# Optimization experiments

Measured on AMD Instinct MI355X. Metric: run time of the kernel, lower is better.

The kernel has to match this reference:

```python
import jax, jax.numpy as jnp
import numpy as np
from jax import lax

B, NAV, HIM, WIM, RH, NF, AE = 16, 36, 120, 160, 512, 4, 37
TEMP = 10.0  # __init__ overrides softmax_temperature to 10
DN = ('NCHW', 'OIHW', 'NCHW')


def _conv(x, w, b, stride, pad, dil, groups):
    y = lax.conv_general_dilated(x, w, window_strides=stride,
                                 padding=[(pad[0], pad[0]), (pad[1], pad[1])],
                                 rhs_dilation=dil, dimension_numbers=DN,
                                 feature_group_count=groups)
    return y + b[None, :, None, None]


def _avgpool(x, k, s):
    y = lax.reduce_window(x, 0.0, lax.add, (1, 1) + k, (1, 1) + s, 'VALID')
    return y / float(k[0] * k[1])


def _conv2_path(x, w1, b1, w2, b2):
    # conv2_1 -> avgpool(3,3) -> conv2_2 -> avgpool(3,9); output [B,3,12]
    y = _conv(x, w1, b1, (5, 7), (0, 0), (10, 10), 1)
    y = _avgpool(y, (3, 3), (3, 3))
    y = _conv(y, w2, b2, (2, 2), (0, 0), (1, 2), 1)
    y = _avgpool(y, (3, 9), (3, 3))
    return y[:, 0]  # squeeze channel -> [B,3,12]


def setup_inputs() -> dict:
    key = jax.random.key(0)
    ks = jax.random.split(key, 24)
    p = lambda k, shape, s=0.02: (jax.random.normal(k, shape) * s).astype(jnp.float32)
    inp = {
        'depth_raw': jax.random.uniform(ks[0], (B, NAV, HIM, WIM), jnp.float32),
        'depth_clip': jax.random.uniform(ks[1], (B, NAV, HIM, WIM), jnp.float32),
        'obj_feat': jax.random.uniform(ks[2], (B, NAV, HIM, WIM), jnp.float32),
        'num_navigable_feat': jax.random.uniform(ks[3], (B, NAV), jnp.float32),
        'pre_action_feat': jax.random.normal(ks[4], (B, AE), jnp.float32),
        'h_0': jax.random.normal(ks[5], (B, RH), jnp.float32),
        'c_0': jax.random.normal(ks[6], (B, RH), jnp.float32),
        'weighted_ctx': jax.random.normal(ks[7], (B, RH), jnp.float32),
        'navigable_index': jax.random.randint(ks[8], (B, 8), 0, NAV),
        # conv1: grouped Conv2d(72 -> 36, k=5, pad=2, groups=36)
        'conv1_w': p(ks[9], (NAV, 2, 5, 5)),
        'conv1_b': p(ks[10], (NAV,)),
        # Dynamic_conv2d: MLP ctx -> filter attention + bank of 4 grouped-filter sets
        'dyn_fc1_w': p(ks[11], (RH // 4, RH)),
        'dyn_fc1_b': p(ks[12], (RH // 4,)),
        'dyn_fc2_w': p(ks[13], (NF, RH // 4)),
        'dyn_fc2_b': p(ks[14], (NF,)),
        'dyn_filters': p(ks[15], (NF, NAV, 2, 5, 5)),
        # conv2_1 / conv2_2: 1->1 channel convs
        'conv2_1_w': p(ks[16], (1, 1, 5, 5)),
        'conv2_1_b': p(ks[17], (1,)),
        'conv2_2_w': p(ks[18], (1, 1, 3, 3)),
        'conv2_2_b': p(ks[19], (1,)),
        # LSTMCell(input=RH+NAV+NF+AE, hidden=RH); gates ordered i,f,g,o
        'lstm_w_ih': p(ks[20], (4 * RH, RH + NAV + NF + AE)),
        'lstm_w_hh': p(ks[21], (4 * RH, RH)),
        'lstm_b_ih': p(ks[22], (4 * RH,)),
        'lstm_b_hh': p(ks[23], (4 * RH,)),
    }
    return inp


def reference(depth_raw, depth_clip, obj_feat, num_navigable_feat, pre_action_feat,
              h_0, c_0, weighted_ctx, navigable_index,
              conv1_w, conv1_b, dyn_fc1_w, dyn_fc1_b, dyn_fc2_w, dyn_fc2_b, dyn_filters,
              conv2_1_w, conv2_1_b, conv2_2_w, conv2_2_b,
              lstm_w_ih, lstm_w_hh, lstm_b_ih, lstm_b_hh):
    # interleave raw/clip depth channels: [B,36,2,H,W] -> [B,72,H,W]
    mtf1 = jnp.stack((depth_raw, depth_clip), axis=2).reshape(B, 2 * NAV, HIM, WIM)
    total_depth = _conv(mtf1, conv1_w, conv1_b, (1, 1), (2, 2), (1, 1), NAV)  # [B,36,H,W]

    attn = jax.nn.softmax(num_navigable_feat, axis=1)  # [B,36]
    pd = total_depth * attn[:, :, None, None]
    po = obj_feat * attn[:, :, None, None]
    mtf2 = jnp.stack((pd, po), axis=2).reshape(B, 2 * NAV, HIM, WIM)

    # dynamic filter conv: ctx-conditioned mixture of filter banks
    hid = jax.nn.relu(weighted_ctx @ dyn_fc1_w.T + dyn_fc1_b)
    dfa = jax.nn.softmax(hid @ dyn_fc2_w.T + dyn_fc2_b, axis=1)  # [B,4]
    kern = jnp.einsum('bf,foikl->boikl', dfa, dyn_filters)  # [B,36,2,5,5]

    def one_sample(xb, kb):
        return lax.conv_general_dilated(xb[None], kb, (1, 1), [(2, 2), (2, 2)],
                                        dimension_numbers=DN,
                                        feature_group_count=NAV)[0]

    tvf = jax.vmap(one_sample)(mtf2, kern)  # [B,36,H,W]

    # panorama assembly: dir i -> row (2 - i//12), col (i%12)
    pano = tvf.reshape(B, 3, 12, HIM, WIM)[:, ::-1]
    pano = pano.transpose(0, 1, 3, 2, 4).reshape(B, 1, 3 * HIM, 12 * WIM)

    vf1 = _conv2_path(pano, conv2_1_w, conv2_1_b, conv2_2_w, conv2_2_b)
    vf2 = _conv2_path(jnp.roll(pano, WIM, axis=3), conv2_1_w, conv2_1_b, conv2_2_w, conv2_2_b)
    vf2 = jnp.roll(vf2, -1, axis=-1)
    vf = (vf1 + vf2) * 0.5
    vf = vf[:, ::-1].reshape(B, NAV)  # flip rows then flatten
    vf = jax.nn.softmax(vf / TEMP, axis=1)

    nav_mask = jnp.zeros((B, NAV), jnp.float32).at[jnp.arange(B)[:, None], navigable_index].set(1.0)

    concat = jnp.concatenate((weighted_ctx, vf, dfa, pre_action_feat), axis=1)
    gates = concat @ lstm_w_ih.T + lstm_b_ih + h_0 @ lstm_w_hh.T + lstm_b_hh
    i, f, g, o = jnp.split(gates, 4, axis=1)
    c_1 = jax.nn.sigmoid(f) * c_0 + jax.nn.sigmoid(i) * jnp.tanh(g)
    h_1 = jax.nn.sigmoid(o) * jnp.tanh(c_1)
    return (h_1, c_1, vf, nav_mask)
```

## Files before the change

kernel.cpp:

```cpp
#include <hip/hip_runtime.h>
#include <math.h>

#define B 16
#define NAV 36
#define HIM 120
#define WIM 160
#define RH 512
#define NF 4
#define AE 37


__global__ __launch_bounds__(128) void k_head(
    const float* __restrict__ nnf, const float* __restrict__ ctx,
    const float* __restrict__ fc1w, const float* __restrict__ fc1b,
    const float* __restrict__ fc2w, const float* __restrict__ fc2b,
    float* __restrict__ attn, float* __restrict__ dfa) {
  int b = blockIdx.x;
  int t = threadIdx.x;
  __shared__ float s_ctx[RH];
  __shared__ float s_v[NAV];
  __shared__ float s_hid[128];
  __shared__ float s_l[NF];
  __shared__ float s_inv[2];

  if (t < NAV) s_v[t] = nnf[b * NAV + t];
  for (int k = t; k < RH; k += 128) s_ctx[k] = ctx[b * RH + k];
  __syncthreads();

  if (t == 0) {
    float m = -1e30f;
    for (int i = 0; i < NAV; i++) m = fmaxf(m, s_v[i]);
    float s = 0.f;
    for (int i = 0; i < NAV; i++) { s_v[i] = expf(s_v[i] - m); s += s_v[i]; }
    s_inv[0] = 1.0f / s;
  }
  float acc = fc1b[t];
  const float* wr = fc1w + t * RH;
  for (int k = 0; k < RH; k++) acc += s_ctx[k] * wr[k];
  s_hid[t] = fmaxf(acc, 0.0f);
  __syncthreads();

  if (t < NAV) attn[b * NAV + t] = s_v[t] * s_inv[0];
  if (t < NF) {
    float a = fc2b[t];
    const float* w2 = fc2w + t * 128;
    for (int k = 0; k < 128; k++) a += s_hid[k] * w2[k];
    s_l[t] = a;
  }
  __syncthreads();
  if (t == 0) {
    float m = fmaxf(fmaxf(s_l[0], s_l[1]), fmaxf(s_l[2], s_l[3]));
    float s = 0.f;
    for (int f = 0; f < NF; f++) { s_l[f] = expf(s_l[f] - m); s += s_l[f]; }
    s_inv[1] = 1.0f / s;
  }
  __syncthreads();
  if (t < NF) dfa[b * NF + t] = s_l[t] * s_inv[1];
}

__global__ __launch_bounds__(192) void k_comp(
    const float* __restrict__ c1w, const float* __restrict__ c1b,
    const float* __restrict__ dynf,
    const float* __restrict__ attn, const float* __restrict__ dfa,
    float* __restrict__ wsC) {
  int bi = blockIdx.x;
  int b = bi / NAV, i = bi - b * NAV;
  int t = threadIdx.x;
  __shared__ float s_kd[50];
  __shared__ float s_w1[50];
  if (t < 50) {
    float a = 0.f;
    for (int f = 0; f < NF; f++) a += dfa[b * NF + f] * dynf[(f * NAV + i) * 50 + t];
    s_kd[t] = a;
    s_w1[t] = c1w[i * 50 + t];
  }
  __syncthreads();
  float attn_bi = attn[bi];
  float* o = wsC + (size_t)bi * 240;
  if (t < 162) {
    int ch = t < 81 ? 0 : 1;
    int uv = t - 81 * ch;
    int u = uv / 9, v = uv - 9 * u;
    float c = 0.f;
    for (int a = 0; a < 5; a++) {
      int cc = u - a; if (cc < 0 || cc > 4) continue;
      for (int bb = 0; bb < 5; bb++) {
        int d = v - bb; if (d < 0 || d > 4) continue;
        c += s_kd[a * 5 + bb] * s_w1[ch * 25 + cc * 5 + d];
      }
    }
    o[ch * 81 + uv] = c * attn_bi;
  } else if (t < 187) {
    o[t] = s_kd[25 + (t - 162)] * attn_bi;
  } else if (t == 187) {
    float s2 = 0.f;
    for (int j = 0; j < 25; j++) s2 += s_kd[j];
    o[187] = attn_bi * c1b[i] * s2;
  }
  if (t < 50) o[188 + t] = s_kd[t];
}

#define LDW 172
__global__ __launch_bounds__(512) void k_conv(
    const float* __restrict__ draw, const float* __restrict__ dclip,
    const float* __restrict__ obj,
    const float* __restrict__ wsC,
    float* __restrict__ cpano) {
  __shared__ __align__(16) float s_raw[24 * LDW];
  __shared__ __align__(16) float s_clip[24 * LDW];
  __shared__ __align__(16) float s_po[20 * LDW];
  __shared__ __align__(16) float s_part[1920];
  __shared__ float s_C[188];

  int t = threadIdx.x;
  int bz = blockIdx.x;
  int half = bz & 1;
  int pi = bz >> 1;
  int b = pi / NAV, i = pi - b * NAV;
  int ybase = 60 * half;

  const size_t plane = (size_t)pi * HIM * WIM;
  const float* rawp = draw + plane;
  const float* clipp = dclip + plane;
  const float* objp = obj + plane;
  int q = i / 12, cw = i - 12 * q;
  float* cpb = cpano + ((size_t)b * 72 + (2 - q) * 24) * 1920 + cw * WIM;

  const float* cp = wsC + (size_t)pi * 240;
  if (t < 188) s_C[t] = cp[t];
  if (t < 384) {
    int ha = t < 192 ? 0 : 1, rem = t - 192 * ha;
    int r = rem >> 3, hc = rem & 7;
    int col = hc < 4 ? hc : 160 + hc;
    (ha ? s_clip : s_raw)[r * LDW + col] = 0.f;
  }
  if (t < 160) {
    int r = t >> 3, hc = t & 7;
    int col = hc < 4 ? hc : 160 + hc;
    s_po[r * LDW + col] = 0.f;
  }

  int prow[2], pg3[2]; bool pra[2];
#pragma unroll
  for (int jj = 0; jj < 2; jj++) {
    int idx = t + 512 * jj;
    pra[jj] = idx < 960;
    prow[jj] = idx / 40;
    pg3[jj] = idx - 40 * prow[jj];
  }
  int vrow[2], vg[2]; bool va[2];
#pragma unroll
  for (int jj = 0; jj < 2; jj++) {
    int idx = t + 512 * jj;
    va[jj] = idx < 800;
    vrow[jj] = idx / 40;
    vg[jj] = idx - 40 * vrow[jj];
  }
  int part = t / 160;
  int pgc = t - 160 * part;
  int row4 = pgc / 40;
  int gc = pgc - 40 * row4;
  int x0 = 4 * gc;
  int rbase = 5 * row4;
  bool cact = (t < 480);
  int rrow4 = t / 40;
  int rg = t - 40 * rrow4;

  for (int tt = 0; tt < 3; tt++) {
    int y0 = ybase + 20 * tt;
    {
      float4 vr[2], vc[2], vo[2];
#pragma unroll
      for (int jj = 0; jj < 2; jj++) {
        int gy = y0 - 4 + prow[jj];
        bool ok = pra[jj] && gy >= 0 && gy < HIM;
        float4 a = {0.f, 0.f, 0.f, 0.f}, c = {0.f, 0.f, 0.f, 0.f};
        if (ok) { a = *(const float4*)(rawp + gy * WIM + 4 * pg3[jj]);
                  c = *(const float4*)(clipp + gy * WIM + 4 * pg3[jj]); }
        vr[jj] = a; vc[jj] = c;
      }
#pragma unroll
      for (int jj = 0; jj < 2; jj++) {
        int gy = y0 - 2 + vrow[jj];
        float4 v = {0.f, 0.f, 0.f, 0.f};
        if (va[jj] && gy >= 0 && gy < HIM)
          v = *(const float4*)(objp + gy * WIM + 4 * vg[jj]);
        vo[jj] = v;
      }
#pragma unroll
      for (int jj = 0; jj < 2; jj++) {
        if (pra[jj]) {
          *(float4*)&s_raw[prow[jj] * LDW + 4 + 4 * pg3[jj]] = vr[jj];
          *(float4*)&s_clip[prow[jj] * LDW + 4 + 4 * pg3[jj]] = vc[jj];
        }
      }
#pragma unroll
      for (int jj = 0; jj < 2; jj++) {
        if (va[jj]) *(float4*)&s_po[vrow[jj] * LDW + 4 + 4 * vg[jj]] = vo[jj];
      }
    }
    __syncthreads();

    if (cact) {
      float a0 = 0.f, a1 = 0.f, a2 = 0.f, a3 = 0.f;
      int ub = rbase + 3 * part;
#pragma unroll
      for (int u = 0; u < 3; u++) {
        const float* rp = &s_raw[(ub + u) * LDW + x0];
        const float* cl = &s_clip[(ub + u) * LDW + x0];
        float rw[12], cc[12];
        *(float4*)&rw[0] = *(const float4*)rp;
        *(float4*)&rw[4] = *(const float4*)(rp + 4);
        *(float4*)&rw[8] = *(const float4*)(rp + 8);
        *(float4*)&cc[0] = *(const float4*)cl;
        *(float4*)&cc[4] = *(const float4*)(cl + 4);
        *(float4*)&cc[8] = *(const float4*)(cl + 8);
        const float* Cr = &s_C[(3 * part + u) * 9];
#pragma unroll
        for (int v = 0; v < 9; v++) {
          float wr = Cr[v], wc = Cr[81 + v];
          a0 += rw[v] * wr + cc[v] * wc;
          a1 += rw[v + 1] * wr + cc[v + 1] * wc;
          a2 += rw[v + 2] * wr + cc[v + 2] * wc;
          a3 += rw[v + 3] * wr + cc[v + 3] * wc;
        }
      }
      int ndd = (part == 2) ? 1 : 2;
      int dd0 = 2 * part;
      for (int dd = 0; dd < ndd; dd++) {
        int dr = dd0 + dd;
        const float* pp = &s_po[(rbase + dr) * LDW + x0];
        float po[12];
        *(float4*)&po[0] = *(const float4*)pp;
        *(float4*)&po[4] = *(const float4*)(pp + 4);
        *(float4*)&po[8] = *(const float4*)(pp + 8);
        const float* Cp = &s_C[162 + dr * 5];
#pragma unroll
        for (int d = 0; d < 5; d++) {
          float w = Cp[d];
          a0 += po[d + 2] * w;
          a1 += po[d + 3] * w;
          a2 += po[d + 4] * w;
          a3 += po[d + 5] * w;
        }
      }
      float4 p4 = {a0, a1, a2, a3};
      *(float4*)&s_part[t * 4] = p4;
    }
    __syncthreads();

    if (t < 160) {
      float4 p0 = *(const float4*)&s_part[(0 * 160 + t) * 4];
      float4 p1 = *(const float4*)&s_part[(1 * 160 + t) * 4];
      float4 p2 = *(const float4*)&s_part[(2 * 160 + t) * 4];
      float c187 = s_C[187];
      float a0 = p0.x + p1.x + p2.x + c187;
      float a1 = p0.y + p1.y + p2.y + c187;
      float a2 = p0.z + p1.z + p2.z + c187;
      float a3 = p0.w + p1.w + p2.w + c187;
      int y = y0 + 5 * rrow4;
      if (y != 0) {
        float* op = cpb + (size_t)(12 * half + 4 * tt + rrow4) * 1920 + 4 * rg;
        if (rg == 0) { op[2] = a2; op[3] = a3; }
        else if (rg == 39) { op[0] = a0; op[1] = a1; }
        else { float4 o4 = {a0, a1, a2, a3}; *(float4*)op = o4; }
      }
    }
  }
}

__global__ __launch_bounds__(256) void k_fix(
    const float* __restrict__ draw, const float* __restrict__ dclip,
    const float* __restrict__ obj,
    const float* __restrict__ c1w, const float* __restrict__ c1b,
    const float* __restrict__ attn, const float* __restrict__ wsC,
    float* __restrict__ cpano) {
  __shared__ float s_top[2][5][168];
  __shared__ float s_L[2][120][13];
  __shared__ float s_R[2][120][13];
  __shared__ float s_pdt[3][168];
  __shared__ float s_pdL[4][120];
  __shared__ float s_pdR[4][120];
  __shared__ float s_w1[50], s_kd[50];

  int bi = blockIdx.x;
  int b = bi / NAV, i = bi - b * NAV;
  int t = threadIdx.x;
  const size_t plane = (size_t)bi * HIM * WIM;
  const float* rawp = draw + plane;
  const float* clipp = dclip + plane;
  const float* objp = obj + plane;
  float attn_bi = attn[bi];
  float bias = c1b[i];

  if (t < 50) { s_w1[t] = c1w[i * 50 + t]; s_kd[t] = wsC[(size_t)bi * 240 + 188 + t]; }
  if (t < 80) { int a = t / 40, rem = t - 40 * a; int r = rem / 8, hc = rem & 7;
    s_top[a][r][hc < 4 ? hc : 160 + hc] = 0.f; }
  else if (t < 104) { int rem = t - 80; int r = rem / 8, hc = rem & 7;
    s_pdt[r][hc < 4 ? hc : 160 + hc] = 0.f; }
  for (int it = t; it < 2 * 2 * 120 * 7; it += 256) {
    int side = it / 1680, rem = it - 1680 * side;
    int a = rem / 840; rem -= 840 * a;
    int row = rem / 7, jj = rem - 7 * row;
    if (side == 0) s_L[a][row][jj < 2 ? jj : 6 + jj] = 0.f;
    else           s_R[a][row][6 + jj] = 0.f;
  }
  for (int it = t; it < 400; it += 256) {
    int a = it / 200, rem = it - 200 * a;
    int r = rem / 40, g = rem - 40 * r;
    const float* src = a ? clipp : rawp;
    *(float4*)&s_top[a][r][4 + 4 * g] = *(const float4*)(src + r * WIM + 4 * g);
  }
  for (int it = t; it < 2 * 2 * 120 * 6; it += 256) {
    int side = it / 1440, rem = it - 1440 * side;
    int a = rem / 720; rem -= 720 * a;
    int row = rem / 6, c = rem - 6 * row;
    const float* src = a ? clipp : rawp;
    if (side == 0) s_L[a][row][2 + c] = src[row * WIM + c];
    else           s_R[a][row][c] = src[row * WIM + 154 + c];
  }
  __syncthreads();

  for (int it = t; it < 480; it += 256) {
    int r = it / 160, x = it - 160 * r;
    float v = 0.f;
#pragma unroll
    for (int c = 0; c < 5; c++) {
      int rr = r - 2 + c;
      if (rr >= 0) {
#pragma unroll
        for (int d = 0; d < 5; d++) {
          int j = 2 + x + d;
          v += s_w1[c * 5 + d] * s_top[0][rr][j] + s_w1[25 + c * 5 + d] * s_top[1][rr][j];
        }
      }
    }
    s_pdt[r][4 + x] = bias + v;
  }
  for (int it = t; it < 460; it += 256) {
    int c = it / 115, y = 3 + (it - 115 * c);
    float v = 0.f;
#pragma unroll
    for (int cp = 0; cp < 5; cp++) {
      int rr = y - 2 + cp;
#pragma unroll
      for (int d = 0; d < 5; d++)
        v += s_w1[cp * 5 + d] * s_L[0][rr][c + d] + s_w1[25 + cp * 5 + d] * s_L[1][rr][c + d];
    }
    s_pdL[c][y] = bias + v;
  }
  for (int it = t; it < 460; it += 256) {
    int c = it / 115, y = 3 + (it - 115 * c);
    float v = 0.f;
#pragma unroll
    for (int cp = 0; cp < 5; cp++) {
      int rr = y - 2 + cp;
#pragma unroll
      for (int d = 0; d < 5; d++)
        v += s_w1[cp * 5 + d] * s_R[0][rr][c + d] + s_w1[25 + cp * 5 + d] * s_R[1][rr][c + d];
    }
    s_pdR[c][y] = bias + v;
  }
  __syncthreads();

  if (t < 252) {
    int y, x;
    if (t < 160) { y = 0; x = t; }
    else {
      int k = t - 160;
      int ri = k >> 2, xi = k & 3;
      y = 5 * (ri + 1);
      x = xi < 2 ? xi : 156 + xi;
    }
    float acc = 0.f;
    if (y == 0) {
#pragma unroll
      for (int a = 2; a < 5; a++)
#pragma unroll
        for (int bb2 = 0; bb2 < 5; bb2++)
          acc += s_kd[a * 5 + bb2] * s_pdt[a - 2][2 + x + bb2];
    } else {
#pragma unroll
      for (int a = 0; a < 5; a++) {
        int ry = y + a - 2;
#pragma unroll
        for (int bb2 = 0; bb2 < 5; bb2++) {
          int q = x + bb2 - 2;
          if (q < 0 || q >= 160) continue;
          float pdv = (q < 4) ? s_pdL[q][ry] : s_pdR[q - 156][ry];
          acc += s_kd[a * 5 + bb2] * pdv;
        }
      }
    }
#pragma unroll
    for (int dd = 0; dd < 5; dd++) {
      int ry = y + dd - 2;
      if (ry < 0 || ry >= HIM) continue;
#pragma unroll
      for (int d = 0; d < 5; d++) {
        int rx = x + d - 2;
        if (rx < 0 || rx >= WIM) continue;
        acc += s_kd[25 + dd * 5 + d] * objp[ry * WIM + rx];
      }
    }
    acc *= attn_bi;
    int q2 = i / 12, cw = i - 12 * q2;
    cpano[((size_t)b * 72 + (2 - q2) * 24 + y / 5) * 1920 + cw * WIM + x] = acc;
  }
}

__global__ __launch_bounds__(256) void k_c21(
    const float* __restrict__ cpano, const float* __restrict__ w21,
    const float* __restrict__ b21, float* __restrict__ y1) {
  __shared__ float s_rows[5][1920];
  int t = threadIdx.x;
  int b = blockIdx.x, oy = blockIdx.y;
  const float* pp = cpano + (size_t)b * 72 * 1920;
  for (int tt = t; tt < 2400; tt += 256) {
    int ky = tt / 480, g = tt - 480 * ky;
    *(float4*)&s_rows[ky][4 * g] = *(const float4*)&pp[(size_t)(oy + 2 * ky) * 1920 + 4 * g];
  }
  float w[25];
#pragma unroll
  for (int k = 0; k < 25; k++) w[k] = w21[k];
  float bb = b21[0];
  __syncthreads();
  for (int tt = t; tt < 538; tt += 256) {
    int p = tt / 269, ox = tt - 269 * p;
    int shift = p ? 1760 : 0;
    float acc = bb;
#pragma unroll
    for (int ky = 0; ky < 5; ky++)
#pragma unroll
      for (int kx = 0; kx < 5; kx++) {
        int X = 7 * ox + 10 * kx + shift;
        if (X >= 1920) X -= 1920;
        acc += w[ky * 5 + kx] * s_rows[ky][X];
      }
    y1[((size_t)(p * B + b) * 64 + oy) * 269 + ox] = acc;
  }
}

__global__ __launch_bounds__(512) void k_tailvf(
    const float* __restrict__ y1, const float* __restrict__ w22,
    const float* __restrict__ b22, const int* __restrict__ nav_idx,
    float* __restrict__ out_vf, float* __restrict__ out_mask) {
  __shared__ float s_y2[2][21][90];
  __shared__ float s_y3[2][10][44];
  __shared__ float s_vf2[2][36];
  __shared__ float s_v[36];
  __shared__ float s_inv;
  int t = threadIdx.x;
  int b = blockIdx.x;
  int p = t >> 8, tp = t & 255;
  const float* yp = y1 + (size_t)(p * B + b) * 64 * 269;
  for (int idx = tp; idx < 21 * 89; idx += 256) {
    int py = idx / 89, px = idx - 89 * py;
    float s = 0.f;
    for (int dy = 0; dy < 3; dy++)
      for (int dx = 0; dx < 3; dx++)
        s += yp[(3 * py + dy) * 269 + 3 * px + dx];
    s_y2[p][py][px] = s * (1.0f / 9.0f);
  }
  __syncthreads();
  for (int idx = tp; idx < 10 * 43; idx += 256) {
    int qy = idx / 43, qx = idx - 43 * qy;
    float a = b22[0];
#pragma unroll
    for (int ky = 0; ky < 3; ky++)
#pragma unroll
      for (int kx = 0; kx < 3; kx++)
        a += w22[ky * 3 + kx] * s_y2[p][2 * qy + ky][2 * qx + 2 * kx];
    s_y3[p][qy][qx] = a;
  }
  __syncthreads();
  if (tp < 36) {
    int uy = tp / 12, ux = tp - 12 * uy;
    float s = 0.f;
    for (int dy = 0; dy < 3; dy++)
      for (int dx = 0; dx < 9; dx++)
        s += s_y3[p][3 * uy + dy][3 * ux + dx];
    s_vf2[p][tp] = s * (1.0f / 27.0f);
  }
  __syncthreads();
  if (t < 36) {
    int u = t / 12, x = t - 12 * u;
    float v1 = s_vf2[0][(2 - u) * 12 + x];
    float v2 = s_vf2[1][(2 - u) * 12 + (x + 1) % 12];
    s_v[t] = 0.5f * (v1 + v2) * 0.1f;
  }
  __syncthreads();
  if (t == 0) {
    float m = -1e30f;
    for (int i = 0; i < 36; i++) m = fmaxf(m, s_v[i]);
    float s = 0.f;
    for (int i = 0; i < 36; i++) { s_v[i] = expf(s_v[i] - m); s += s_v[i]; }
    s_inv = 1.0f / s;
  }
  __syncthreads();
  if (t < 36) {
    out_vf[b * 36 + t] = s_v[t] * s_inv;
    float m = 0.f;
    for (int e = 0; e < 8; e++)
      if (nav_idx[b * 8 + e] == t) m = 1.0f;
    out_mask[b * 36 + t] = m;
  }
}

__global__ __launch_bounds__(256) void k_lstm(
    const float* __restrict__ ctx, const float* __restrict__ vf,
    const float* __restrict__ dfa, const float* __restrict__ pre,
    const float* __restrict__ h0, const float* __restrict__ c0,
    const float* __restrict__ wih, const float* __restrict__ whh,
    const float* __restrict__ bih, const float* __restrict__ bhh,
    float* __restrict__ h1, float* __restrict__ c1) {
  __shared__ float s_cat[B][1104];
  __shared__ float s_g[4][16];
  int t = threadIdx.x;
  int u = blockIdx.x;
  int g = t >> 6, l = t & 63;
  for (int idx = t; idx < B * 589; idx += 256) {
    int b = idx / 589, k = idx - 589 * b;
    float v;
    if (k < 512) v = ctx[b * 512 + k];
    else if (k < 548) v = vf[b * 36 + (k - 512)];
    else if (k < 552) v = dfa[b * 4 + (k - 548)];
    else v = pre[b * 37 + (k - 552)];
    s_cat[b][k] = v;
  }
  for (int idx = t; idx < B * 512; idx += 256) {
    int b = idx >> 9, k = idx & 511;
    s_cat[b][592 + k] = h0[b * 512 + k];
  }
  __syncthreads();
  int j = (g << 9) + u;
  float acc[B];
#pragma unroll
  for (int b = 0; b < B; b++) acc[b] = 0.f;
  const float* wi = wih + (size_t)j * 589;
#pragma unroll
  for (int it = 0; it < 3; it++) {
    int c = l + 64 * it;
    if (c < 147) {
      int k = 4 * c;
      float w0 = wi[k], w1 = wi[k + 1], w2 = wi[k + 2], w3 = wi[k + 3];
#pragma unroll
      for (int b = 0; b < B; b++) {
        float4 cc = *(const float4*)&s_cat[b][k];
        acc[b] += cc.x * w0 + cc.y * w1 + cc.z * w2 + cc.w * w3;
      }
    }
  }
  if (l == 0) {
    float w = wi[588];
#pragma unroll
    for (int b = 0; b < B; b++) acc[b] += w * s_cat[b][588];
  }
  const float* wh = whh + (size_t)j * 512;
#pragma unroll
  for (int it = 0; it < 2; it++) {
    int k = 4 * (l + 64 * it);
    float4 w4 = *(const float4*)&wh[k];
#pragma unroll
    for (int b = 0; b < B; b++) {
      float4 cc = *(const float4*)&s_cat[b][592 + k];
      acc[b] += cc.x * w4.x + cc.y * w4.y + cc.z * w4.z + cc.w * w4.w;
    }
  }
#pragma unroll
  for (int off = 1; off < 64; off <<= 1)
#pragma unroll
    for (int b = 0; b < B; b++) acc[b] += __shfl_xor(acc[b], off);
  if (l == 0) {
    float bb = bih[j] + bhh[j];
#pragma unroll
    for (int b = 0; b < B; b++) s_g[g][b] = acc[b] + bb;
  }
  __syncthreads();
  if (t < 16) {
    float gi = s_g[0][t], gf = s_g[1][t], gg = s_g[2][t], go = s_g[3][t];
    float c_old = c0[t * 512 + u];
    float si = 1.0f / (1.0f + expf(-gi));
    float sf = 1.0f / (1.0f + expf(-gf));
    float so = 1.0f / (1.0f + expf(-go));
    float cn = sf * c_old + si * tanhf(gg);
    h1[t * 512 + u] = so * tanhf(cn);
    c1[t * 512 + u] = cn;
  }
}

extern "C" void kernel_launch(void* const* d_in, const int* in_sizes, int n_in,
                              void* d_out, int out_size, void* d_ws, size_t ws_size,
                              hipStream_t stream) {
  const float* depth_raw  = (const float*)d_in[0];
  const float* depth_clip = (const float*)d_in[1];
  const float* obj_feat   = (const float*)d_in[2];
  const float* nnf        = (const float*)d_in[3];
  const float* pre        = (const float*)d_in[4];
  const float* h0         = (const float*)d_in[5];
  const float* c0         = (const float*)d_in[6];
  const float* ctx        = (const float*)d_in[7];
  const int*   nav_idx    = (const int*)d_in[8];
  const float* c1w        = (const float*)d_in[9];
  const float* c1b        = (const float*)d_in[10];
  const float* fc1w       = (const float*)d_in[11];
  const float* fc1b       = (const float*)d_in[12];
  const float* fc2w       = (const float*)d_in[13];
  const float* fc2b       = (const float*)d_in[14];
  const float* dynf       = (const float*)d_in[15];
  const float* w21        = (const float*)d_in[16];
  const float* b21        = (const float*)d_in[17];
  const float* w22        = (const float*)d_in[18];
  const float* b22        = (const float*)d_in[19];
  const float* wih        = (const float*)d_in[20];
  const float* whh        = (const float*)d_in[21];
  const float* bih        = (const float*)d_in[22];
  const float* bhh        = (const float*)d_in[23];

  float* ws = (float*)d_ws;
  float* attn   = ws;
  float* dfa    = ws + 576;
  float* y1     = ws + 1792;
  float* cpano  = ws + 552704;
  float* wsC    = ws + 2764544;

  float* out = (float*)d_out;
  float* out_h1   = out;
  float* out_c1   = out + 8192;
  float* out_vf   = out + 16384;
  float* out_mask = out + 16960;

  k_head<<<B, 128, 0, stream>>>(nnf, ctx, fc1w, fc1b, fc2w, fc2b, attn, dfa);
  k_comp<<<B * NAV, 192, 0, stream>>>(c1w, c1b, dynf, attn, dfa, wsC);
  k_conv<<<B * NAV * 2, 512, 0, stream>>>(depth_raw, depth_clip, obj_feat, wsC, cpano);
  k_fix<<<B * NAV, 256, 0, stream>>>(depth_raw, depth_clip, obj_feat,
                                     c1w, c1b, attn, wsC, cpano);
  k_c21<<<dim3(B, 64), 256, 0, stream>>>(cpano, w21, b21, y1);
  k_tailvf<<<B, 512, 0, stream>>>(y1, w22, b22, nav_idx, out_vf, out_mask);
  k_lstm<<<RH, 256, 0, stream>>>(ctx, out_vf, dfa, pre, h0, c0,
                                 wih, whh, bih, bhh, out_h1, out_c1);
}
```

Measured before the change: 127.8 us.

## Read conv inputs directly from global memory instead of LDS tiles

Rewrites k_conv so each thread computes one output group by loading raw, clip and object rows straight from global memory (float4), dropping the LDS staging buffers, partial-sum reduction and block barriers. The grid moves to four 256-thread blocks per plane, and each thread accumulates the full 9-row and 5-row stencils itself. This removes shared-memory traffic and syncs and raises occupancy, in exchange for redundant global and cache loads across overlapping rows and per-thread edge handling.

```diff
diff --git a/kernel.cpp b/kernel.cpp
--- a/kernel.cpp
+++ b/kernel.cpp
@@ -100,173 +100,81 @@
   if (t < 50) o[188 + t] = s_kd[t];
 }
 
-#define LDW 172
-__global__ __launch_bounds__(512) void k_conv(
+__global__ __launch_bounds__(256) void k_conv(
     const float* __restrict__ draw, const float* __restrict__ dclip,
     const float* __restrict__ obj,
     const float* __restrict__ wsC,
     float* __restrict__ cpano) {
-  __shared__ __align__(16) float s_raw[24 * LDW];
-  __shared__ __align__(16) float s_clip[24 * LDW];
-  __shared__ __align__(16) float s_po[20 * LDW];
-  __shared__ __align__(16) float s_part[1920];
   __shared__ float s_C[188];
-
-  int t = threadIdx.x;
-  int bz = blockIdx.x;
-  int half = bz & 1;
-  int pi = bz >> 1;
+  int bk = blockIdx.x;
+  int pi = bk >> 2, sub = bk & 3;
   int b = pi / NAV, i = pi - b * NAV;
-  int ybase = 60 * half;
-
-  const size_t plane = (size_t)pi * HIM * WIM;
+  int t = threadIdx.x;
+  if (t < 188) s_C[t] = wsC[(size_t)pi * 240 + t];
+  __syncthreads();
+
+  int item = sub * 256 + t;
+  if (item >= 960) return;
+  int crow = item / 40, g = item - 40 * crow;
+  int y = 5 * crow;
+  if (y == 0) return;
+  int x0 = 4 * g;
+  bool mlo = (g == 0), mhi = (g == 39);
+
+  const size_t plane = (size_t)pi * (HIM * WIM);
   const float* rawp = draw + plane;
   const float* clipp = dclip + plane;
   const float* objp = obj + plane;
+
+  float a0 = s_C[187], a1 = a0, a2 = a0, a3 = a0;
+  const float4 z4 = {0.f, 0.f, 0.f, 0.f};
+
+  const float* rb = rawp + (y - 4) * WIM + x0 - 4;
+  const float* cb = clipp + (y - 4) * WIM + x0 - 4;
+#pragma unroll
+  for (int u = 0; u < 9; u++) {
+    float rw[12], cc[12];
+    const float* rp = rb + u * WIM;
+    const float* cp = cb + u * WIM;
+    *(float4*)&rw[0] = mlo ? z4 : *(const float4*)rp;
+    *(float4*)&rw[4] = *(const float4*)(rp + 4);
+    *(float4*)&rw[8] = mhi ? z4 : *(const float4*)(rp + 8);
+    *(float4*)&cc[0] = mlo ? z4 : *(const float4*)cp;
+    *(float4*)&cc[4] = *(const float4*)(cp + 4);
+    *(float4*)&cc[8] = mhi ? z4 : *(const float4*)(cp + 8);
+    const float* Cr = &s_C[u * 9];
+#pragma unroll
+    for (int v = 0; v < 9; v++) {
+      float wr = Cr[v], wc = Cr[81 + v];
+      a0 += rw[v] * wr + cc[v] * wc;
+      a1 += rw[v + 1] * wr + cc[v + 1] * wc;
+      a2 += rw[v + 2] * wr + cc[v + 2] * wc;
+      a3 += rw[v + 3] * wr + cc[v + 3] * wc;
+    }
+  }
+  const float* ob = objp + (y - 2) * WIM + x0 - 4;
+#pragma unroll
+  for (int dd = 0; dd < 5; dd++) {
+    float po[12];
+    const float* pp = ob + dd * WIM;
+    *(float4*)&po[0] = mlo ? z4 : *(const float4*)pp;
+    *(float4*)&po[4] = *(const float4*)(pp + 4);
+    *(float4*)&po[8] = mhi ? z4 : *(const float4*)(pp + 8);
+    const float* Cp = &s_C[162 + dd * 5];
+#pragma unroll
+    for (int d = 0; d < 5; d++) {
+      float w = Cp[d];
+      a0 += po[d + 2] * w;
+      a1 += po[d + 3] * w;
+      a2 += po[d + 4] * w;
+      a3 += po[d + 5] * w;
+    }
+  }
   int q = i / 12, cw = i - 12 * q;
-  float* cpb = cpano + ((size_t)b * 72 + (2 - q) * 24) * 1920 + cw * WIM;
-
-  const float* cp = wsC + (size_t)pi * 240;
-  if (t < 188) s_C[t] = cp[t];
-  if (t < 384) {
-    int ha = t < 192 ? 0 : 1, rem = t - 192 * ha;
-    int r = rem >> 3, hc = rem & 7;
-    int col = hc < 4 ? hc : 160 + hc;
-    (ha ? s_clip : s_raw)[r * LDW + col] = 0.f;
-  }
-  if (t < 160) {
-    int r = t >> 3, hc = t & 7;
-    int col = hc < 4 ? hc : 160 + hc;
-    s_po[r * LDW + col] = 0.f;
-  }
-
-  int prow[2], pg3[2]; bool pra[2];
-#pragma unroll
-  for (int jj = 0; jj < 2; jj++) {
-    int idx = t + 512 * jj;
-    pra[jj] = idx < 960;
-    prow[jj] = idx / 40;
-    pg3[jj] = idx - 40 * prow[jj];
-  }
-  int vrow[2], vg[2]; bool va[2];
-#pragma unroll
-  for (int jj = 0; jj < 2; jj++) {
-    int idx = t + 512 * jj;
-    va[jj] = idx < 800;
-    vrow[jj] = idx / 40;
-    vg[jj] = idx - 40 * vrow[jj];
-  }
-  int part = t / 160;
-  int pgc = t - 160 * part;
-  int row4 = pgc / 40;
-  int gc = pgc - 40 * row4;
-  int x0 = 4 * gc;
-  int rbase = 5 * row4;
-  bool cact = (t < 480);
-  int rrow4 = t / 40;
-  int rg = t - 40 * rrow4;
-
-  for (int tt = 0; tt < 3; tt++) {
-    int y0 = ybase + 20 * tt;
-    {
-      float4 vr[2], vc[2], vo[2];
-#pragma unroll
-      for (int jj = 0; jj < 2; jj++) {
-        int gy = y0 - 4 + prow[jj];
-        bool ok = pra[jj] && gy >= 0 && gy < HIM;
-        float4 a = {0.f, 0.f, 0.f, 0.f}, c = {0.f, 0.f, 0.f, 0.f};
-        if (ok) { a = *(const float4*)(rawp + gy * WIM + 4 * pg3[jj]);
-                  c = *(const float4*)(clipp + gy * WIM + 4 * pg3[jj]); }
-        vr[jj] = a; vc[jj] = c;
-      }
-#pragma unroll
-      for (int jj = 0; jj < 2; jj++) {
-        int gy = y0 - 2 + vrow[jj];
-        float4 v = {0.f, 0.f, 0.f, 0.f};
-        if (va[jj] && gy >= 0 && gy < HIM)
-          v = *(const float4*)(objp + gy * WIM + 4 * vg[jj]);
-        vo[jj] = v;
-      }
-#pragma unroll
-      for (int jj = 0; jj < 2; jj++) {
-        if (pra[jj]) {
-          *(float4*)&s_raw[prow[jj] * LDW + 4 + 4 * pg3[jj]] = vr[jj];
-          *(float4*)&s_clip[prow[jj] * LDW + 4 + 4 * pg3[jj]] = vc[jj];
-        }
-      }
-#pragma unroll
-      for (int jj = 0; jj < 2; jj++) {
-        if (va[jj]) *(float4*)&s_po[vrow[jj] * LDW + 4 + 4 * vg[jj]] = vo[jj];
-      }
-    }
-    __syncthreads();
-
-    if (cact) {
-      float a0 = 0.f, a1 = 0.f, a2 = 0.f, a3 = 0.f;
-      int ub = rbase + 3 * part;
-#pragma unroll
-      for (int u = 0; u < 3; u++) {
-        const float* rp = &s_raw[(ub + u) * LDW + x0];
-        const float* cl = &s_clip[(ub + u) * LDW + x0];
-        float rw[12], cc[12];
-        *(float4*)&rw[0] = *(const float4*)rp;
-        *(float4*)&rw[4] = *(const float4*)(rp + 4);
-        *(float4*)&rw[8] = *(const float4*)(rp + 8);
-        *(float4*)&cc[0] = *(const float4*)cl;
-        *(float4*)&cc[4] = *(const float4*)(cl + 4);
-        *(float4*)&cc[8] = *(const float4*)(cl + 8);
-        const float* Cr = &s_C[(3 * part + u) * 9];
-#pragma unroll
-        for (int v = 0; v < 9; v++) {
-          float wr = Cr[v], wc = Cr[81 + v];
-          a0 += rw[v] * wr + cc[v] * wc;
-          a1 += rw[v + 1] * wr + cc[v + 1] * wc;
-          a2 += rw[v + 2] * wr + cc[v + 2] * wc;
-          a3 += rw[v + 3] * wr + cc[v + 3] * wc;
-        }
-      }
-      int ndd = (part == 2) ? 1 : 2;
-      int dd0 = 2 * part;
-      for (int dd = 0; dd < ndd; dd++) {
-        int dr = dd0 + dd;
-        const float* pp = &s_po[(rbase + dr) * LDW + x0];
-        float po[12];
-        *(float4*)&po[0] = *(const float4*)pp;
-        *(float4*)&po[4] = *(const float4*)(pp + 4);
-        *(float4*)&po[8] = *(const float4*)(pp + 8);
-        const float* Cp = &s_C[162 + dr * 5];
-#pragma unroll
-        for (int d = 0; d < 5; d++) {
-          float w = Cp[d];
-          a0 += po[d + 2] * w;
-          a1 += po[d + 3] * w;
-          a2 += po[d + 4] * w;
-          a3 += po[d + 5] * w;
-        }
-      }
-      float4 p4 = {a0, a1, a2, a3};
-      *(float4*)&s_part[t * 4] = p4;
-    }
-    __syncthreads();
-
-    if (t < 160) {
-      float4 p0 = *(const float4*)&s_part[(0 * 160 + t) * 4];
-      float4 p1 = *(const float4*)&s_part[(1 * 160 + t) * 4];
-      float4 p2 = *(const float4*)&s_part[(2 * 160 + t) * 4];
-      float c187 = s_C[187];
-      float a0 = p0.x + p1.x + p2.x + c187;
-      float a1 = p0.y + p1.y + p2.y + c187;
-      float a2 = p0.z + p1.z + p2.z + c187;
-      float a3 = p0.w + p1.w + p2.w + c187;
-      int y = y0 + 5 * rrow4;
-      if (y != 0) {
-        float* op = cpb + (size_t)(12 * half + 4 * tt + rrow4) * 1920 + 4 * rg;
-        if (rg == 0) { op[2] = a2; op[3] = a3; }
-        else if (rg == 39) { op[0] = a0; op[1] = a1; }
-        else { float4 o4 = {a0, a1, a2, a3}; *(float4*)op = o4; }
-      }
-    }
-  }
+  float* op = cpano + ((size_t)b * 72 + (2 - q) * 24 + crow) * 1920 + cw * WIM + x0;
+  if (mlo) { op[2] = a2; op[3] = a3; }
+  else if (mhi) { op[0] = a0; op[1] = a1; }
+  else { float4 o4 = {a0, a1, a2, a3}; *(float4*)op = o4; }
 }
 
 __global__ __launch_bounds__(256) void k_fix(
@@ -632,7 +540,7 @@
 
   k_head<<<B, 128, 0, stream>>>(nnf, ctx, fc1w, fc1b, fc2w, fc2b, attn, dfa);
   k_comp<<<B * NAV, 192, 0, stream>>>(c1w, c1b, dynf, attn, dfa, wsC);
-  k_conv<<<B * NAV * 2, 512, 0, stream>>>(depth_raw, depth_clip, obj_feat, wsC, cpano);
+  k_conv<<<B * NAV * 4, 256, 0, stream>>>(depth_raw, depth_clip, obj_feat, wsC, cpano);
   k_fix<<<B * NAV, 256, 0, stream>>>(depth_raw, depth_clip, obj_feat,
                                      c1w, c1b, attn, wsC, cpano);
   k_c21<<<dim3(B, 64), 256, 0, stream>>>(cpano, w21, b21, y1);
```

Measured after the change: 198.4 us. 55.3% more time.
